# Performance work log

Measured on AMD Instinct MI355X. Metric: run time of the kernel, lower is better.

The kernel has to match this reference:

```python
import jax, jax.numpy as jnp
import numpy as np

N, D, K = 4096, 1024, 32
MARGIN = 0.3
OP_TYPE = "weighty"


def setup_inputs() -> dict:
    key = jax.random.key(0)
    k1, k2, k3, k4, k5 = jax.random.split(key, 5)
    return {
        "inputs": jax.random.normal(k1, (N, D), jnp.float32),
        "prediction": jax.random.normal(k2, (N, K), jnp.float32),
        "targets": jax.random.randint(k3, (N,), 0, K),
        "true_targets": jax.random.randint(k4, (N,), 0, K),
        "prob": jax.random.uniform(k5, (N,), jnp.float32),
        "threshold": jnp.float32(0.5),
    }


def _weighty(d1, d2, pair_type, op_type):
    # vectorized translation of weighty_new
    if op_type == "mean":
        return (d1 + d2) / 2.0
    if op_type == "max":
        return jnp.maximum(d1, d2)
    if op_type == "min":
        return jnp.minimum(d1, d2)
    if op_type == "max-min":
        return jnp.maximum(d1, d2) if pair_type == 1 else jnp.minimum(d1, d2)
    # op_type == 'weighty'
    if pair_type == 1:
        e1, e2 = jnp.exp(d1), jnp.exp(d2)
        return (e1 * d1 + e2 * d2) / (e1 + e2)
    e1, e2 = jnp.exp(-d1), jnp.exp(-d2)
    return (e1 * d1 + e2 * d2) / (e1 + e2 + 1e-6)


def reference(inputs, prediction, targets, true_targets, prob, threshold):
    n = inputs.shape[0]
    rows = jnp.arange(n)
    # pairwise euclidean dist (GEMM-based, matches addmm_ formulation)
    sq = jnp.sum(inputs * inputs, axis=1)
    dist = sq[:, None] + sq[None, :] - 2.0 * (inputs @ inputs.T)
    dist = jnp.sqrt(jnp.clip(dist, 1e-12, None))  # [n, n]

    same = targets[:, None] == targets[None, :]
    conf = prob >= threshold

    # negatives sorted ascending by dist; positives sorted descending by dist
    neg_order = jnp.argsort(jnp.where(~same, dist, jnp.inf), axis=1)   # [n,n]
    pos_order = jnp.argsort(jnp.where(same, -dist, jnp.inf), axis=1)   # [n,n]
    hp = pos_order[:, 0]   # hardest positive (max dist)
    hn = neg_order[:, 0]   # hardest negative (min dist)
    d_ap = dist[rows, hp]
    d_an = dist[rows, hn]

    cp = prob[hp] >= threshold
    cn = prob[hn] >= threshold
    fn = jnp.argmax(prediction, axis=1)[hn] == targets  # hard neg is a false negative

    # neg re-selection: ranks 1..10 first with prob>=t, else rank 11 (loop_cnt cap 10)
    neg_cand = neg_order[:, 1:12]                       # [n,11]
    ok_n = prob[neg_cand] >= threshold
    sel_n = jnp.where(ok_n[:, :10].any(axis=1), jnp.argmax(ok_n[:, :10], axis=1), 10)
    d_nn = dist[rows, neg_cand[rows, sel_n]]

    # pos re-selection: descending ranks 1..5 first with prob>=t, else rank 6 (loop_cnt cap 5)
    pos_cand = pos_order[:, 1:7]                        # [n,6]
    ok_p = prob[pos_cand] >= threshold
    sel_p = jnp.where(ok_p[:, :5].any(axis=1), jnp.argmax(ok_p[:, :5], axis=1), 5)
    d_np = dist[rows, pos_cand[rows, sel_p]]

    w1 = _weighty(d_ap, d_an, 1, OP_TYPE)
    w0 = _weighty(d_ap, d_an, 0, OP_TYPE)

    case_b = cp & (~cn) & fn                 # confident pos, unconfident FN neg
    case_cd = (~cp) & (cn | (~fn))           # unconfident pos branches that re-select pos
    inv = (~cp) & (~cn) & fn                 # inverse loss branch

    ap = jnp.where(case_b, w1, jnp.where(case_cd, d_np, d_ap))
    an = jnp.where(case_b, d_nn, jnp.where(case_cd, w0, d_an))

    per = jnp.where(inv,
                    jax.nn.relu(an - ap + MARGIN),
                    jax.nn.relu(ap - an + MARGIN))
    conff = conf.astype(per.dtype)
    cnt = jnp.sum(conf.astype(jnp.int32))
    loss = jnp.where(cnt > 0, jnp.sum(per * conff) / jnp.maximum(cnt, 1).astype(per.dtype), 0.0)
    correct = jnp.sum(((an >= ap) & conf).astype(jnp.int32))
    return loss, correct, cnt
```

## Files before the change

kernel.cpp:

```cpp
#include <hip/hip_runtime.h>
#include <hip/hip_bf16.h>
#include <stdint.h>

typedef _Float16 half8 __attribute__((ext_vector_type(8)));
typedef _Float16 half4 __attribute__((ext_vector_type(4)));
typedef float f32x4 __attribute__((ext_vector_type(4)));
typedef unsigned short ushort8v __attribute__((ext_vector_type(8)));
typedef unsigned short ushort4v __attribute__((ext_vector_type(4)));
typedef unsigned long long u64;

#define N_ROWS 4096
#define DIM 1024
#define KCLS 32
#define MARGIN_F 0.3f

typedef const __attribute__((address_space(1))) void GASV;
typedef __attribute__((address_space(3))) void LASV;

__device__ __forceinline__ void gload_lds16(const void* g, void* l) {
    __builtin_amdgcn_global_load_lds((GASV*)g, (LASV*)l, 16, 0, 0);
}

__global__ __launch_bounds__(256) void prep_kernel(
    const float* __restrict__ inputs, const float* __restrict__ prediction,
    _Float16* __restrict__ xh, float* __restrict__ sq, int* __restrict__ pred_cls)
{
    int wid = threadIdx.x >> 6, lane = threadIdx.x & 63;
    int r = blockIdx.x * 4 + wid;
    const float* row = inputs + (size_t)r * DIM;
    _Float16* hrow = xh + (size_t)r * DIM;
    float s = 0.f;
#pragma unroll
    for (int c = 0; c < 4; ++c) {
        int idx = lane * 4 + c * 256;
        float4 v = *(const float4*)(row + idx);
        s += v.x * v.x + v.y * v.y + v.z * v.z + v.w * v.w;
        half4 h;
        h.x = (_Float16)v.x; h.y = (_Float16)v.y;
        h.z = (_Float16)v.z; h.w = (_Float16)v.w;
        *(half4*)(hrow + idx) = h;
    }
#pragma unroll
    for (int off = 32; off; off >>= 1) s += __shfl_xor(s, off);

    u64 key = 0ull;
    if (lane < KCLS) {
        unsigned b = __float_as_uint(prediction[(size_t)r * KCLS + lane]);
        unsigned u = (b & 0x80000000u) ? ~b : (b | 0x80000000u);
        key = ((u64)u << 32) | (unsigned)(KCLS - 1 - lane);
    }
#pragma unroll
    for (int off = 32; off; off >>= 1) {
        u64 o = __shfl_xor(key, off);
        if (o > key) key = o;
    }
    if (lane == 0) {
        sq[r] = s;
        pred_cls[r] = KCLS - 1 - (int)(key & 0xFFFFFFFFu);
    }
}

__global__ __launch_bounds__(512) void gemm_kernel(
    const _Float16* __restrict__ X, const float* __restrict__ sq,
    const int* __restrict__ targets,
    unsigned short* __restrict__ out, int mode, int rb0)
{
    __shared__ __align__(16) _Float16 As[128 * 64];
    __shared__ __align__(16) _Float16 Bs[128 * 64];
    int tid = threadIdx.x;

    int bx, by;
    bool diag = false, mirror = false;
    if (mode == 0) {
        int u = ((int)blockIdx.x & 7) * 66 + ((int)blockIdx.x >> 3);
        int t_ = (int)((sqrtf(8.f * u + 1.f) - 1.f) * 0.5f);
        while ((t_ + 1) * (t_ + 2) / 2 <= u) ++t_;
        while (t_ * (t_ + 1) / 2 > u) --t_;
        by = t_;
        bx = u - t_ * (t_ + 1) / 2;
        diag = (bx == by);
        mirror = !diag;
    } else {
        int nwg = gridDim.x;
        int q = nwg >> 3;
        int swz = ((int)blockIdx.x & 7) * q + ((int)blockIdx.x >> 3);
        int nbx = nwg / 32;
        bx = swz % nbx;
        by = swz / nbx;
    }

    int rs = tid >> 3;
    int ss = tid & 7;
    int srcslot = ss ^ (rs & 7);
    const _Float16* gA = X + (size_t)(rb0 + bx * 128 + rs) * DIM + srcslot * 8;
    const _Float16* gB = X + (size_t)(by * 128 + rs) * DIM + srcslot * 8;
    _Float16* lA = As + tid * 8;
    _Float16* lB = Bs + tid * 8;

    int wid = tid >> 6, lane = tid & 63;
    int wr = (wid >> 2) * 64, wc = (wid & 3) * 32;
    int fr = lane & 15, q4 = lane >> 4;

    f32x4 acc[4][2];
#pragma unroll
    for (int m = 0; m < 4; ++m)
#pragma unroll
        for (int n = 0; n < 2; ++n) acc[m][n] = (f32x4){0.f, 0.f, 0.f, 0.f};

    for (int k0 = 0; k0 < DIM; k0 += 64) {
#pragma unroll
        for (int p = 0; p < 2; ++p) {
            gload_lds16(gA + k0 + (size_t)(p * 64) * DIM, lA + p * 4096);
            if (!diag) gload_lds16(gB + k0 + (size_t)(p * 64) * DIM, lB + p * 4096);
        }
        __syncthreads();
        const _Float16* Bsrc = diag ? As : Bs;
#pragma unroll
        for (int ks = 0; ks < 2; ++ks) {
            half8 a[4], b[2];
#pragma unroll
            for (int m = 0; m < 4; ++m) {
                int row = wr + m * 16 + fr;
                int s = (ks * 4 + q4) ^ (row & 7);
                a[m] = *(const half8*)(As + row * 64 + s * 8);
            }
#pragma unroll
            for (int n = 0; n < 2; ++n) {
                int brow = wc + n * 16 + fr;
                int s = (ks * 4 + q4) ^ (brow & 7);
                b[n] = *(const half8*)(Bsrc + brow * 64 + s * 8);
            }
#pragma unroll
            for (int m = 0; m < 4; ++m)
#pragma unroll
                for (int n = 0; n < 2; ++n)
                    acc[m][n] = __builtin_amdgcn_mfma_f32_16x16x32_f16(a[m], b[n], acc[m][n], 0, 0, 0);
        }
        __syncthreads();
    }

    int rbase = rb0 + bx * 128 + wr + q4 * 4;
    float sqr_[4][4];
    int trr[4][4];
#pragma unroll
    for (int m = 0; m < 4; ++m)
#pragma unroll
        for (int q = 0; q < 4; ++q) {
            sqr_[m][q] = sq[rbase + m * 16 + q];
            trr[m][q] = targets[rbase + m * 16 + q];
        }

#pragma unroll
    for (int n = 0; n < 2; ++n) {
        int col = by * 128 + wc + n * 16 + fr;
        float sqc = sq[col];
        int tc = targets[col];
#pragma unroll
        for (int m = 0; m < 4; ++m) {
            int row0 = rbase + m * 16;
            ushort4v hv;
#pragma unroll
            for (int q = 0; q < 4; ++q) {
                float d2v = fmaxf(sqr_[m][q] + sqc - 2.f * acc[m][n][q], 1e-12f);
                _Float16 h = (_Float16)d2v;
                unsigned short hb = __builtin_bit_cast(unsigned short, h);
                hb = (unsigned short)(hb | ((trr[m][q] == tc) ? 0x8000u : 0u));
                hv[q] = hb;
                out[(size_t)(row0 + q) * N_ROWS + col] = hb;
            }
            if (mirror)
                *(ushort4v*)&out[(size_t)col * N_ROWS + row0] = hv;
        }
    }
}

__global__ __launch_bounds__(256) void select_kernel(
    const unsigned short* __restrict__ dot,
    const int* __restrict__ targets, const float* __restrict__ prob,
    const int* __restrict__ pred_cls, const float* __restrict__ thr_p,
    int rb0, float* __restrict__ per_term, int* __restrict__ corr_flag)
{
    __shared__ unsigned Tn[4], Tp[4];
    __shared__ unsigned negCand[64];
    __shared__ unsigned posCand[64];
    __shared__ unsigned cnts[2];
    __shared__ unsigned sN[12], sP[7];
    __shared__ unsigned red[4];
    __shared__ unsigned bcast;

    int t = threadIdx.x, lane = t & 63, w = t >> 6;
    int rloc = blockIdx.x, r = rb0 + rloc;
    const unsigned short* drow = dot + (size_t)rloc * N_ROWS;

    if (t < 64) { negCand[t] = 0xFFFFFFFFu; posCand[t] = 0u; }
    if (t < 2) cnts[t] = 0u;

    unsigned short hb[16];
    unsigned mneg = 0xFFFFFFFFu, mpos = 0u;
    {
        ushort8v v0 = *(const ushort8v*)(drow + t * 8);
        ushort8v v1 = *(const ushort8v*)(drow + 2048 + t * 8);
#pragma unroll
        for (int j = 0; j < 8; ++j) {
            unsigned b = v0[j]; hb[j] = (unsigned short)b;
            if (b & 0x8000u) mpos = mpos > b ? mpos : b; else mneg = mneg < b ? mneg : b;
        }
#pragma unroll
        for (int j = 0; j < 8; ++j) {
            unsigned b = v1[j]; hb[8 + j] = (unsigned short)b;
            if (b & 0x8000u) mpos = mpos > b ? mpos : b; else mneg = mneg < b ? mneg : b;
        }
    }

    unsigned T3 = 0xFFFFFFFFu, m = mneg;
#pragma unroll
    for (int rd = 0; rd < 3; ++rd) {
        unsigned b = m;
#pragma unroll
        for (int off = 32; off; off >>= 1) {
            unsigned o = __shfl_xor(b, off);
            b = o < b ? o : b;
        }
        T3 = b;
        if (m == b) m = 0xFFFFFFFFu;
    }
    unsigned P2 = 0u, mp = mpos;
#pragma unroll
    for (int rd = 0; rd < 2; ++rd) {
        unsigned b = mp;
#pragma unroll
        for (int off = 32; off; off >>= 1) {
            unsigned o = __shfl_xor(b, off);
            b = o > b ? o : b;
        }
        P2 = b;
        if (mp == b) mp = 0u;
    }
    if (lane == 0) { Tn[w] = T3; Tp[w] = P2; }
    __syncthreads();

    unsigned TnB = Tn[0];
    TnB = Tn[1] > TnB ? Tn[1] : TnB;
    TnB = Tn[2] > TnB ? Tn[2] : TnB;
    TnB = Tn[3] > TnB ? Tn[3] : TnB;
    unsigned TpB = Tp[0];
    TpB = Tp[1] < TpB ? Tp[1] : TpB;
    TpB = Tp[2] < TpB ? Tp[2] : TpB;
    TpB = Tp[3] < TpB ? Tp[3] : TpB;

#pragma unroll
    for (int j = 0; j < 16; ++j) {
        int col = (j < 8) ? (t * 8 + j) : (2048 + t * 8 + (j - 8));
        unsigned b = hb[j];
        if (!(b & 0x8000u) && b <= TnB) {
            unsigned s = atomicAdd(&cnts[0], 1u);
            if (s < 64u) negCand[s] = (b << 16) | (unsigned)col;
        }
        if ((b & 0x8000u) && b >= TpB) {
            unsigned s = atomicAdd(&cnts[1], 1u);
            if (s < 64u) posCand[s] = (b << 16) | (unsigned)(N_ROWS - 1 - col);
        }
    }
    __syncthreads();

    bool fb = (cnts[0] > 64u) || (cnts[1] > 64u);

    if (!fb) {
        if (w == 0) {
            unsigned v = negCand[lane];
#pragma unroll
            for (int k = 2; k <= 64; k <<= 1) {
#pragma unroll
                for (int j = 32; j; j >>= 1) {
                    if (j >= k) continue;
                    unsigned o = __shfl_xor(v, j);
                    bool up = (lane & k) == 0;
                    bool small = (lane & j) == 0;
                    bool keepmin = (small == up);
                    unsigned lo = v < o ? v : o, hi = v < o ? o : v;
                    v = keepmin ? lo : hi;
                }
            }
            if (lane < 12) sN[lane] = v;
        } else if (w == 1) {
            unsigned v = ~posCand[lane];
#pragma unroll
            for (int k = 2; k <= 64; k <<= 1) {
#pragma unroll
                for (int j = 32; j; j >>= 1) {
                    if (j >= k) continue;
                    unsigned o = __shfl_xor(v, j);
                    bool up = (lane & k) == 0;
                    bool small = (lane & j) == 0;
                    bool keepmin = (small == up);
                    unsigned lo = v < o ? v : o, hi = v < o ? o : v;
                    v = keepmin ? lo : hi;
                }
            }
            if (lane < 7) sP[lane] = ~v;
        }
    } else {
        unsigned remN = 0, remP = 0;
        for (int rd = 0; rd < 12; ++rd) {
            unsigned best = 0xFFFFFFFFu;
#pragma unroll
            for (int j = 0; j < 16; ++j) {
                int col = (j < 8) ? (t * 8 + j) : (2048 + t * 8 + (j - 8));
                unsigned b = hb[j];
                bool valid = !(b & 0x8000u) && !((remN >> j) & 1u);
                unsigned nk = valid ? ((b << 16) | (unsigned)col) : 0xFFFFFFFFu;
                best = nk < best ? nk : best;
            }
#pragma unroll
            for (int off = 32; off; off >>= 1) {
                unsigned o = __shfl_xor(best, off);
                best = o < best ? o : best;
            }
            if (lane == 0) red[w] = best;
            __syncthreads();
            if (t == 0) {
                unsigned b0 = red[0];
                b0 = red[1] < b0 ? red[1] : b0;
                b0 = red[2] < b0 ? red[2] : b0;
                b0 = red[3] < b0 ? red[3] : b0;
                sN[rd] = b0; bcast = b0;
            }
            __syncthreads();
            unsigned b0 = bcast;
#pragma unroll
            for (int j = 0; j < 16; ++j) {
                int col = (j < 8) ? (t * 8 + j) : (2048 + t * 8 + (j - 8));
                if ((((unsigned)hb[j] << 16) | (unsigned)col) == b0) remN |= 1u << j;
            }
            __syncthreads();
        }
        for (int rd = 0; rd < 7; ++rd) {
            unsigned best = 0u;
#pragma unroll
            for (int j = 0; j < 16; ++j) {
                int col = (j < 8) ? (t * 8 + j) : (2048 + t * 8 + (j - 8));
                unsigned b = hb[j];
                bool valid = (b & 0x8000u) && !((remP >> j) & 1u);
                unsigned pk = valid ? ((b << 16) | (unsigned)(N_ROWS - 1 - col)) : 0u;
                best = pk > best ? pk : best;
            }
#pragma unroll
            for (int off = 32; off; off >>= 1) {
                unsigned o = __shfl_xor(best, off);
                best = o > best ? o : best;
            }
            if (lane == 0) red[w] = best;
            __syncthreads();
            if (t == 0) {
                unsigned b0 = red[0];
                b0 = red[1] > b0 ? red[1] : b0;
                b0 = red[2] > b0 ? red[2] : b0;
                b0 = red[3] > b0 ? red[3] : b0;
                sP[rd] = b0; bcast = b0;
            }
            __syncthreads();
            unsigned b0 = bcast;
#pragma unroll
            for (int j = 0; j < 16; ++j) {
                int col = (j < 8) ? (t * 8 + j) : (2048 + t * 8 + (j - 8));
                if ((((unsigned)hb[j] << 16) | (unsigned)(N_ROWS - 1 - col)) == b0) remP |= 1u << j;
            }
            __syncthreads();
        }
    }
    __syncthreads();

    if (w == 0) {
        float thr = *thr_p;
        int tr = targets[r];
        unsigned kN = (lane < 12) ? sN[lane] : 0xFFFFFFFFu;
        unsigned kP = (lane >= 32 && lane < 39) ? sP[lane - 32] : 0u;
        int idxN = (int)(kN & 0xFFFFu) & (N_ROWS - 1);
        int idxP = (N_ROWS - 1 - (int)(kP & 0xFFFFu)) & (N_ROWS - 1);
        bool confN = (lane < 12) && kN != 0xFFFFFFFFu && (prob[idxN] >= thr);
        bool confP = (lane >= 32 && lane < 39) && kP != 0u && (prob[idxP] >= thr);
        u64 balN = __ballot(confN);
        u64 balP = __ballot(confP);

        u64 mN_ = balN & 0x7FEull;
        int selN = mN_ ? (__ffsll(mN_) - 1) : 11;
        unsigned dnn_b = __shfl(kN >> 16, selN);
        u64 mP_ = balP & (0x3Eull << 32);
        int selP = mP_ ? (__ffsll(mP_) - 1) : 38;
        unsigned dnp_b = __shfl(kP >> 16, selP);
        unsigned dap_b = __shfl(kP >> 16, 32);

        if (lane == 0) {
            auto h2f = [](unsigned b16) -> float {
                unsigned short us = (unsigned short)(b16 & 0x7FFFu);
                _Float16 h = __builtin_bit_cast(_Float16, us);
                return (float)h;
            };
            float d_ap = sqrtf(h2f(dap_b));
            float d_an = sqrtf(h2f(kN >> 16));
            int hn = idxN;
            bool cp = (balP >> 32) & 1ull;
            bool cn = balN & 1ull;
            bool fn = (pred_cls[hn] == tr);
            float d_nn = sqrtf(h2f(dnn_b));
            float d_np = sqrtf(h2f(dnp_b));

            float e1p = __expf(d_ap), e2p = __expf(d_an);
            float w1 = (e1p * d_ap + e2p * d_an) / (e1p + e2p);
            float e1n = __expf(-d_ap), e2n = __expf(-d_an);
            float w0 = (e1n * d_ap + e2n * d_an) / (e1n + e2n + 1e-6f);
            bool case_b = cp && !cn && fn;
            bool case_cd = !cp && (cn || !fn);
            bool inv = !cp && !cn && fn;
            float ap = case_b ? w1 : (case_cd ? d_np : d_ap);
            float an = case_b ? d_nn : (case_cd ? w0 : d_an);
            float per = inv ? fmaxf(an - ap + MARGIN_F, 0.f)
                            : fmaxf(ap - an + MARGIN_F, 0.f);
            per_term[r] = per;
            corr_flag[r] = (an >= ap) ? 1 : 0;
        }
    }
}

__global__ __launch_bounds__(256) void finalize_kernel(
    const float* __restrict__ per_term, const int* __restrict__ corr_flag,
    const float* __restrict__ prob, const float* __restrict__ thr_p,
    float* __restrict__ out)
{
    __shared__ float sred[4]; __shared__ int cred[4]; __shared__ int nred[4];
    float thr = *thr_p;
    int t = threadIdx.x, lane = t & 63, wid = t >> 6;
    float s = 0.f; int c = 0, n = 0;
    for (int i = t; i < N_ROWS; i += 256) {
        if (prob[i] >= thr) {
            s += per_term[i];
            c += corr_flag[i];
            n += 1;
        }
    }
#pragma unroll
    for (int off = 32; off; off >>= 1) {
        s += __shfl_xor(s, off);
        c += __shfl_xor(c, off);
        n += __shfl_xor(n, off);
    }
    if (lane == 0) { sred[wid] = s; cred[wid] = c; nred[wid] = n; }
    __syncthreads();
    if (t == 0) {
        float ss = sred[0] + sred[1] + sred[2] + sred[3];
        int cc = cred[0] + cred[1] + cred[2] + cred[3];
        int nn = nred[0] + nred[1] + nred[2] + nred[3];
        float loss = (nn > 0) ? ss / (float)nn : 0.f;
        out[0] = loss;
        out[1] = (float)cc;
        out[2] = (float)nn;
    }
}

extern "C" void kernel_launch(void* const* d_in, const int* in_sizes, int n_in,
                              void* d_out, int out_size, void* d_ws, size_t ws_size,
                              hipStream_t stream)
{
    const float* inputs     = (const float*)d_in[0];
    const float* prediction = (const float*)d_in[1];
    const int*   targets    = (const int*)d_in[2];
    const float* prob       = (const float*)d_in[4];
    const float* thr        = (const float*)d_in[5];
    float* out = (float*)d_out;

    char* ws = (char*)d_ws;
    size_t off = 0;
    auto alloc = [&](size_t bytes) -> char* {
        char* p = ws + off;
        off = (off + bytes + 255) & ~(size_t)255;
        return p;
    };
    _Float16* xh     = (_Float16*)alloc((size_t)N_ROWS * DIM * sizeof(_Float16));
    float* sq        = (float*)alloc((size_t)N_ROWS * 4);
    int*   pred_cls  = (int*)alloc((size_t)N_ROWS * 4);
    float* per_term  = (float*)alloc((size_t)N_ROWS * 4);
    int*   corr_flag = (int*)alloc((size_t)N_ROWS * 4);

    size_t avail = (ws_size > off) ? (ws_size - off) : 0;
    size_t rowbytes = (size_t)N_ROWS * 2;
    int RB = 128;
    while (RB * 2 <= N_ROWS && (size_t)(RB * 2) * rowbytes <= avail) RB *= 2;
    unsigned short* dotbuf = (unsigned short*)alloc((size_t)RB * rowbytes);

    hipLaunchKernelGGL(prep_kernel, dim3(N_ROWS / 4), dim3(256), 0, stream,
                       inputs, prediction, xh, sq, pred_cls);
    if (RB == N_ROWS) {
        hipLaunchKernelGGL(gemm_kernel, dim3(528), dim3(512), 0, stream,
                           xh, sq, targets, dotbuf, 0, 0);
        hipLaunchKernelGGL(select_kernel, dim3(N_ROWS), dim3(256), 0, stream,
                           dotbuf, targets, prob, pred_cls, thr, 0,
                           per_term, corr_flag);
    } else {
        for (int rb0 = 0; rb0 < N_ROWS; rb0 += RB) {
            hipLaunchKernelGGL(gemm_kernel, dim3((RB / 128) * 32), dim3(512), 0, stream,
                               xh, sq, targets, dotbuf, 1, rb0);
            hipLaunchKernelGGL(select_kernel, dim3(RB), dim3(256), 0, stream,
                               dotbuf, targets, prob, pred_cls, thr, rb0,
                               per_term, corr_flag);
        }
    }
    hipLaunchKernelGGL(finalize_kernel, dim3(1), dim3(256), 0, stream,
                       per_term, corr_flag, prob, thr, out);
}
```

Before: 76.15 us.

## Double-buffer LDS tiles in GEMM with async global-to-LDS prefetch

Converts the GEMM main loop into a two-stage software pipeline. Each K tile is loaded into one of two LDS buffers while the other buffer is being consumed by MFMA, using a vmcnt wait and raw barriers in place of __syncthreads. The goal is to hide global load latency behind compute. It also removes the diagonal-tile special case, so diagonal blocks now load B redundantly. LDS use doubles, to 64KB per block, which may reduce occupancy.

```diff
diff --git a/kernel.cpp b/kernel.cpp
--- a/kernel.cpp
+++ b/kernel.cpp
@@ -65,12 +65,12 @@
     const int* __restrict__ targets,
     unsigned short* __restrict__ out, int mode, int rb0)
 {
-    __shared__ __align__(16) _Float16 As[128 * 64];
-    __shared__ __align__(16) _Float16 Bs[128 * 64];
+    __shared__ __align__(16) _Float16 As[2 * 128 * 64];
+    __shared__ __align__(16) _Float16 Bs[2 * 128 * 64];
     int tid = threadIdx.x;
 
     int bx, by;
-    bool diag = false, mirror = false;
+    bool mirror = false;
     if (mode == 0) {
         int u = ((int)blockIdx.x & 7) * 66 + ((int)blockIdx.x >> 3);
         int t_ = (int)((sqrtf(8.f * u + 1.f) - 1.f) * 0.5f);
@@ -78,8 +78,7 @@
         while (t_ * (t_ + 1) / 2 > u) --t_;
         by = t_;
         bx = u - t_ * (t_ + 1) / 2;
-        diag = (bx == by);
-        mirror = !diag;
+        mirror = (bx != by);
     } else {
         int nwg = gridDim.x;
         int q = nwg >> 3;
@@ -107,14 +106,17 @@
 #pragma unroll
         for (int n = 0; n < 2; ++n) acc[m][n] = (f32x4){0.f, 0.f, 0.f, 0.f};
 
-    for (int k0 = 0; k0 < DIM; k0 += 64) {
+    auto STAGE = [&](int buf, int t) {
+        int k0 = t * 64;
 #pragma unroll
         for (int p = 0; p < 2; ++p) {
-            gload_lds16(gA + k0 + (size_t)(p * 64) * DIM, lA + p * 4096);
-            if (!diag) gload_lds16(gB + k0 + (size_t)(p * 64) * DIM, lB + p * 4096);
-        }
-        __syncthreads();
-        const _Float16* Bsrc = diag ? As : Bs;
+            gload_lds16(gA + k0 + (size_t)(p * 64) * DIM, lA + buf * 8192 + p * 4096);
+            gload_lds16(gB + k0 + (size_t)(p * 64) * DIM, lB + buf * 8192 + p * 4096);
+        }
+    };
+    auto COMPUTE = [&](int buf) {
+        const _Float16* Ac = As + buf * 8192;
+        const _Float16* Bc = Bs + buf * 8192;
 #pragma unroll
         for (int ks = 0; ks < 2; ++ks) {
             half8 a[4], b[2];
@@ -122,13 +124,13 @@
             for (int m = 0; m < 4; ++m) {
                 int row = wr + m * 16 + fr;
                 int s = (ks * 4 + q4) ^ (row & 7);
-                a[m] = *(const half8*)(As + row * 64 + s * 8);
+                a[m] = *(const half8*)(Ac + row * 64 + s * 8);
             }
 #pragma unroll
             for (int n = 0; n < 2; ++n) {
                 int brow = wc + n * 16 + fr;
                 int s = (ks * 4 + q4) ^ (brow & 7);
-                b[n] = *(const half8*)(Bsrc + brow * 64 + s * 8);
+                b[n] = *(const half8*)(Bc + brow * 64 + s * 8);
             }
 #pragma unroll
             for (int m = 0; m < 4; ++m)
@@ -136,8 +138,27 @@
                 for (int n = 0; n < 2; ++n)
                     acc[m][n] = __builtin_amdgcn_mfma_f32_16x16x32_f16(a[m], b[n], acc[m][n], 0, 0, 0);
         }
-        __syncthreads();
-    }
+    };
+
+    STAGE(0, 0);
+    STAGE(1, 1);
+
+    int cur = 0;
+    for (int t = 0; t < 15; ++t) {
+        asm volatile("s_waitcnt vmcnt(4)" ::: "memory");
+        __builtin_amdgcn_s_barrier();
+        __builtin_amdgcn_sched_barrier(0);
+        COMPUTE(cur);
+        __builtin_amdgcn_sched_barrier(0);
+        __builtin_amdgcn_s_barrier();
+        __builtin_amdgcn_sched_barrier(0);
+        if (t + 2 < 16) STAGE(cur, t + 2);
+        cur ^= 1;
+    }
+    asm volatile("s_waitcnt vmcnt(0)" ::: "memory");
+    __builtin_amdgcn_s_barrier();
+    __builtin_amdgcn_sched_barrier(0);
+    COMPUTE(cur);
 
     int rbase = rb0 + bx * 128 + wr + q4 * 4;
     float sqr_[4][4];
```

Measured after the change: 70.50 us (median of 3 runs). 1.08x faster.
